# Performance work log

Measured on AMD Instinct MI355X. Metric: run time of the kernel, lower is better.

Reference implementation:

```python
import jax, jax.numpy as jnp
import numpy as np

STRIDES = (8, 16, 32, 64, 128)
NUM_CLASSES = 80
TOPK = 1000
CONF_THRESH = 0.05
NMS_THRESH = 0.6
IMG_H = IMG_W = 2048
CLASS_OFFSET = 100000.0  # > any box coordinate, makes different-class boxes disjoint


def _level_decode(cls, reg, ctn, scale, stride):
    # cls: [1,C,H,W], reg: [1,4,H,W], ctn: [1,1,H,W]
    C, H, W = cls.shape[1], cls.shape[2], cls.shape[3]
    cls = jnp.transpose(cls[0], (1, 2, 0)).reshape(-1, C)       # [HW, C]
    reg = jnp.transpose(reg[0], (1, 2, 0)).reshape(-1, 4)       # [HW, 4]
    reg = jax.nn.relu(reg * scale) * stride                      # Scale + relu + stride
    ctn = jnp.transpose(ctn[0], (1, 2, 0)).reshape(-1, 1)       # [HW, 1]
    prob = jnp.sqrt(jax.nn.sigmoid(cls) * jax.nn.sigmoid(ctn))  # [HW, C]
    scores = prob.max(axis=-1)
    labels = prob.argmax(axis=-1)
    ys, xs = jnp.meshgrid(jnp.arange(H), jnp.arange(W), indexing='ij')
    anchors = (jnp.stack([xs, ys], axis=-1).reshape(-1, 2).astype(cls.dtype) + 0.5) * stride
    if scores.shape[0] > TOPK:
        scores, idx = jax.lax.top_k(scores, TOPK)
        labels, reg, anchors = labels[idx], reg[idx], anchors[idx]
    # decode (l,t,r,b) deltas around anchor centers -> (x1,y1,x2,y2)
    boxes = jnp.concatenate([anchors - reg[:, :2], anchors + reg[:, 2:]], axis=-1)
    return scores, labels, boxes


def _nms_keep(boxes, scores, valid, thresh):
    # Sequential greedy NMS, same math as the numpy loop in RTEFCOS.nms.
    order = jnp.argsort(-jnp.where(valid, scores, -jnp.inf))
    b = boxes[order]
    v = valid[order]
    x1, y1, x2, y2 = b[:, 0], b[:, 1], b[:, 2], b[:, 3]
    areas = (x2 - x1) * (y2 - y1)
    n = b.shape[0]
    pos = jnp.arange(n)

    def body(i, keep):
        xx1 = jnp.maximum(x1[i], x1)
        yy1 = jnp.maximum(y1[i], y1)
        xx2 = jnp.minimum(x2[i], x2)
        yy2 = jnp.minimum(y2[i], y2)
        inter = jnp.maximum(1e-10, xx2 - xx1) * jnp.maximum(1e-10, yy2 - yy1)
        ovr = inter / (areas[i] + areas - inter + 1e-14)
        suppress = (ovr > thresh) & (pos > i) & keep[i]
        return keep & (~suppress)

    keep_sorted = jax.lax.fori_loop(0, n, body, v)
    return jnp.zeros(n, dtype=bool).at[order].set(keep_sorted)


def reference(cls0, reg0, ctn0, cls1, reg1, ctn1, cls2, reg2, ctn2,
              cls3, reg3, ctn3, cls4, reg4, ctn4, scales):
    levels = [(cls0, reg0, ctn0), (cls1, reg1, ctn1), (cls2, reg2, ctn2),
              (cls3, reg3, ctn3), (cls4, reg4, ctn4)]
    all_s, all_l, all_b = [], [], []
    for lv, (c, r, t) in enumerate(levels):
        s, l, b = _level_decode(c, r, t, scales[lv], STRIDES[lv])
        all_s.append(s); all_l.append(l); all_b.append(b)
    scores = jnp.concatenate(all_s)   # [M]
    labels = jnp.concatenate(all_l)   # [M]
    bboxes = jnp.concatenate(all_b)   # [M, 4]
    valid = scores >= CONF_THRESH     # conf filter as mask (static shapes)
    # class-wise NMS via coordinate-offset trick: boxes of different classes
    # never overlap, so one greedy pass == per-class greedy passes.
    boxes_off = bboxes + labels[:, None].astype(bboxes.dtype) * CLASS_OFFSET
    keep = _nms_keep(boxes_off, scores, valid, NMS_THRESH)
    bboxes = bboxes / jnp.array([IMG_W, IMG_H, IMG_W, IMG_H], dtype=bboxes.dtype)
    bboxes = jnp.clip(bboxes, 0.0, 1.0)
    return bboxes, scores, labels, keep


def setup_inputs():
    key = jax.random.key(0)
    ks = jax.random.split(key, len(STRIDES))
    inp = {}
    for lv, stride in enumerate(STRIDES):
        H = IMG_H // stride
        W = IMG_W // stride
        k1, k2, k3 = jax.random.split(ks[lv], 3)
        inp[f"cls{lv}"] = jax.random.normal(k1, (1, NUM_CLASSES, H, W), jnp.float32)
        inp[f"reg{lv}"] = jax.random.uniform(k2, (1, 4, H, W), jnp.float32)
        inp[f"ctn{lv}"] = jax.random.normal(k3, (1, 1, H, W), jnp.float32)
    inp["scales"] = jnp.ones((5,), jnp.float32)
    return inp
```

## Files before the change

### kernel.cpp

```cpp
#include <hip/hip_runtime.h>
#include <math.h>

#define TOTAL_ANCHORS 87296
#define NTOPK 87040
#define NSEL 4256
#define NWORDS 67
#define NPAD   4288
#define MAXROUNDS 4300
#define CANDMAX 8192
#define NBIN 32768
#define NSLAB 8

__device__ __forceinline__ float sigmoidf_(float x) {
    return 1.0f / (1.0f + expf(-x));
}
__device__ __forceinline__ unsigned int f2s(float f) {
    unsigned int u = __float_as_uint(f);
    return u ^ ((u >> 31) ? 0xFFFFFFFFu : 0x80000000u);
}
__device__ __forceinline__ float s2f(unsigned int k) {
    unsigned int u = (k & 0x80000000u) ? (k ^ 0x80000000u) : ~k;
    return __uint_as_float(u);
}
__device__ __forceinline__ void level_of(int g, int& lv, int& base, int& W, int& stride) {
    if (g < 65536)      { lv = 0; base = 0;     W = 256; stride = 8;   }
    else if (g < 81920) { lv = 1; base = 65536; W = 128; stride = 16;  }
    else if (g < 86016) { lv = 2; base = 81920; W = 64;  stride = 32;  }
    else if (g < 87040) { lv = 3; base = 86016; W = 32;  stride = 64;  }
    else                { lv = 4; base = 87040; W = 16;  stride = 128; }
}

struct InPtrs {
    const float* cls[5];
    const float* reg[5];
    const float* ctn[5];
    const float* scales;
};

__global__ __launch_bounds__(256) void cmax_kernel(InPtrs in,
        unsigned long long* __restrict__ cmax2) {
    int a = blockIdx.x * 256 + threadIdx.x;
    int cg = blockIdx.y;
    int lv, base, W, stride;
    level_of(a, lv, base, W, stride);
    (void)stride;
    int p = a - base;
    int HW = W * W;
    const float* cls = in.cls[lv];
    float sctn = sigmoidf_(in.ctn[lv][p]);
    int c0 = cg * 8;
    float v[8];
    #pragma unroll
    for (int k = 0; k < 8; ++k) v[k] = cls[(c0 + k) * HW + p];
    unsigned long long best = 0ull;
    #pragma unroll
    for (int k = 0; k < 8; ++k) {
        float pr = sqrtf(__fmul_rn(sigmoidf_(v[k]), sctn));
        unsigned long long key = ((unsigned long long)f2s(pr) << 32)
                               | (unsigned long long)(255 - (c0 + k));
        best = (key > best) ? key : best;
    }
    cmax2[(size_t)cg * TOTAL_ANCHORS + a] = best;
}

__global__ __launch_bounds__(256) void decode2_kernel(InPtrs in,
        const unsigned long long* __restrict__ cmax2,
        unsigned long long* __restrict__ keys, float* __restrict__ scores,
        int* __restrict__ labels, float4* __restrict__ boxes) {
    int g = blockIdx.x * 256 + threadIdx.x;
    int lv, base, W, stride;
    level_of(g, lv, base, W, stride);
    int p = g - base;
    int HW = W * W;
    int x = p & (W - 1);
    int y = p / W;
    unsigned long long mk = 0ull;
    #pragma unroll
    for (int cg = 0; cg < 10; ++cg) {
        unsigned long long v = cmax2[(size_t)cg * TOTAL_ANCHORS + g];
        mk = (v > mk) ? v : mk;
    }
    float best = s2f((unsigned int)(mk >> 32));
    int lbl = 255 - (int)(mk & 0xFFull);
    float scale = in.scales[lv];
    float fs = (float)stride;
    const float* rg = in.reg[lv];
    float r0 = __fmul_rn(fmaxf(__fmul_rn(rg[0 * HW + p], scale), 0.0f), fs);
    float r1 = __fmul_rn(fmaxf(__fmul_rn(rg[1 * HW + p], scale), 0.0f), fs);
    float r2 = __fmul_rn(fmaxf(__fmul_rn(rg[2 * HW + p], scale), 0.0f), fs);
    float r3 = __fmul_rn(fmaxf(__fmul_rn(rg[3 * HW + p], scale), 0.0f), fs);
    float ax = __fmul_rn(__fadd_rn((float)x, 0.5f), fs);
    float ay = __fmul_rn(__fadd_rn((float)y, 0.5f), fs);
    float4 b;
    b.x = __fsub_rn(ax, r0);
    b.y = __fsub_rn(ay, r1);
    b.z = __fadd_rn(ax, r2);
    b.w = __fadd_rn(ay, r3);
    scores[g] = best;
    labels[g] = lbl;
    boxes[g]  = b;
    keys[g] = (mk & 0xFFFFFFFF00000000ull)
            | (unsigned long long)(unsigned int)(~(unsigned int)p);
}

__global__ __launch_bounds__(1024) void hist_kernel(
        const unsigned long long* __restrict__ keys,
        unsigned int* __restrict__ slab) {
    __shared__ unsigned int h[NBIN / 2];
    const int starts[NSLAB] = {0, 16384, 32768, 49152, 65536, 73728, 81920, 86016};
    const int ends[NSLAB]   = {16384, 32768, 49152, 65536, 73728, 81920, 86016, 87040};
    const int tid = threadIdx.x;
    for (int i = tid; i < NBIN / 2; i += 1024) h[i] = 0u;
    __syncthreads();
    const int s = starts[blockIdx.x], e = ends[blockIdx.x];
    for (int i = s + tid; i < e; i += 1024) {
        unsigned int bin = (unsigned int)(keys[i] >> 48) & 0x7FFFu;
        atomicAdd(&h[bin >> 1], 1u << ((bin & 1u) << 4));
    }
    __syncthreads();
    unsigned int* out = slab + blockIdx.x * (NBIN / 2);
    for (int i = tid; i < NBIN / 2; i += 1024) out[i] = h[i];
}

__global__ __launch_bounds__(1024) void select_kernel(
        const unsigned int* __restrict__ slab, unsigned int* __restrict__ thr,
        unsigned int* __restrict__ cnt) {
    const int lvl = blockIdx.x;
    const int slabS[4] = {0, 4, 6, 7};
    const int slabE[4] = {4, 6, 7, 8};
    const int tid = threadIdx.x;
    if (lvl == 0 && tid < 128) cnt[tid] = 0u;
    __shared__ unsigned int csum[1024];
    unsigned int s = 0;
    for (int sb = slabS[lvl]; sb < slabE[lvl]; ++sb) {
        const unsigned int* A = slab + sb * (NBIN / 2);
        #pragma unroll 4
        for (int w = tid * 16; w < tid * 16 + 16; ++w) {
            unsigned int v = A[w];
            s += (v & 0xFFFFu) + (v >> 16);
        }
    }
    csum[tid] = s;
    __syncthreads();
    for (int off = 1; off < 1024; off <<= 1) {
        unsigned int v = csum[tid] + ((tid + off < 1024) ? csum[tid + off] : 0u);
        __syncthreads();
        csum[tid] = v;
        __syncthreads();
    }
    unsigned int incl = csum[tid];
    unsigned int incl1 = (tid == 1023) ? 0u : csum[tid + 1];
    if (incl >= 1000u && incl1 < 1000u) {
        unsigned int running = incl1;
        for (int b = tid * 32 + 31; b >= tid * 32; --b) {
            unsigned int c = 0;
            for (int sb = slabS[lvl]; sb < slabE[lvl]; ++sb) {
                unsigned int v = slab[sb * (NBIN / 2) + (b >> 1)];
                c += (v >> ((b & 1) << 4)) & 0xFFFFu;
            }
            running += c;
            if (running >= 1000u) { thr[lvl] = (unsigned int)b; break; }
        }
    }
}

__global__ __launch_bounds__(1024) void gather_kernel(
        const unsigned long long* __restrict__ keys,
        const unsigned int* __restrict__ thr,
        unsigned long long* __restrict__ cand, unsigned int* __restrict__ cnt) {
    int g = blockIdx.x * 1024 + threadIdx.x;
    int lvl;
    if (g < 65536)      lvl = 0;
    else if (g < 81920) lvl = 1;
    else if (g < 86016) lvl = 2;
    else                lvl = 3;
    unsigned long long k = keys[g];
    bool pass = (((unsigned int)(k >> 48)) & 0x7FFFu) >= thr[lvl];
    __shared__ unsigned int woff[16];
    __shared__ unsigned int base_;
    const int wave = threadIdx.x >> 6, lane = threadIdx.x & 63;
    unsigned long long m = __ballot(pass);
    if (lane == 0) woff[wave] = (unsigned int)__popcll(m);
    __syncthreads();
    if (threadIdx.x == 0) {
        unsigned int tot = 0;
        #pragma unroll
        for (int w = 0; w < 16; ++w) { unsigned int c = woff[w]; woff[w] = tot; tot += c; }
        base_ = atomicAdd(&cnt[lvl << 5], tot);
    }
    __syncthreads();
    if (pass) {
        unsigned int pos = base_ + woff[wave]
                         + (unsigned int)__popcll(m & ((1ull << lane) - 1ull));
        if (pos < CANDMAX) cand[(lvl << 13) + pos] = k;
    }
}

__global__ __launch_bounds__(1024) void finalsort_kernel(
        const unsigned long long* __restrict__ cand,
        const unsigned int* __restrict__ cnt,
        unsigned long long* __restrict__ sel) {
    const int lvl = blockIdx.x;
    const int tid = threadIdx.x;
    __shared__ unsigned long long sk[CANDMAX];
    int n = (int)cnt[lvl << 5];
    if (n > CANDMAX) n = CANDMAX;
    int P = 1024;
    while (P < n) P <<= 1;
    for (int i = tid; i < P; i += 1024)
        sk[i] = (i < n) ? cand[(lvl << 13) + i] : 0ull;
    __syncthreads();
    for (int kk = 2; kk <= P; kk <<= 1) {
        for (int j = kk >> 1; j > 0; j >>= 1) {
            for (int i = tid; i < P; i += 1024) {
                int ixj = i ^ j;
                if (ixj > i) {
                    unsigned long long a = sk[i], b = sk[ixj];
                    bool sw = ((i & kk) == 0) ? (a < b) : (a > b);
                    if (sw) { sk[i] = b; sk[ixj] = a; }
                }
            }
            __syncthreads();
        }
    }
    if (tid < 1000) sel[lvl * 1000 + tid] = sk[tid];
}

#define PEND_VEC 3216
__global__ __launch_bounds__(256) void fin_kernel(
        const unsigned long long* __restrict__ sel,
        const float* __restrict__ scores, const int* __restrict__ labels,
        const float4* __restrict__ boxes, float* __restrict__ out,
        float4* __restrict__ entbox, float* __restrict__ entarea,
        int* __restrict__ entvalid, unsigned long long* __restrict__ ekeyG,
        float4* __restrict__ pendzero) {
    int pos = blockIdx.x * 256 + threadIdx.x;
    if (pos < PEND_VEC) pendzero[pos] = make_float4(0.f, 0.f, 0.f, 0.f);
    if (pos >= NSEL) return;
    int g;
    if (pos < 4000) {
        int lv = pos / 1000;
        const int offs_[4] = {0, 65536, 81920, 86016};
        unsigned long long key = sel[pos];
        unsigned int p = ~((unsigned int)(key & 0xFFFFFFFFull));
        g = offs_[lv] + (int)p;
    } else {
        g = 87040 + (pos - 4000);
    }
    float sc = scores[g];
    int lb = labels[g];
    float4 bx = boxes[g];
    const float inv = 1.0f / 2048.0f;
    out[pos * 4 + 0] = fminf(fmaxf(__fmul_rn(bx.x, inv), 0.0f), 1.0f);
    out[pos * 4 + 1] = fminf(fmaxf(__fmul_rn(bx.y, inv), 0.0f), 1.0f);
    out[pos * 4 + 2] = fminf(fmaxf(__fmul_rn(bx.z, inv), 0.0f), 1.0f);
    out[pos * 4 + 3] = fminf(fmaxf(__fmul_rn(bx.w, inv), 0.0f), 1.0f);
    out[17024 + pos] = sc;
    out[21280 + pos] = (float)lb;
    out[25536 + pos] = 0.0f;
    float off = __fmul_rn((float)lb, 100000.0f);
    float4 eb;
    eb.x = __fadd_rn(bx.x, off); eb.y = __fadd_rn(bx.y, off);
    eb.z = __fadd_rn(bx.z, off); eb.w = __fadd_rn(bx.w, off);
    entbox[pos] = eb;
    entarea[pos] = __fmul_rn(__fsub_rn(eb.z, eb.x), __fsub_rn(eb.w, eb.y));
    int valid = (sc >= 0.05f) ? 1 : 0;
    entvalid[pos] = valid;
    float effs = valid ? sc : -INFINITY;
    ekeyG[pos] = ((unsigned long long)f2s(effs) << 32) | (unsigned int)(~(unsigned int)pos);
}

__device__ __forceinline__ int count_greater(const unsigned long long* A, int n,
                                             unsigned long long x) {
    int lo = 0, hi = n;
    while (lo < hi) { int m = (lo + hi) >> 1; if (A[m] > x) lo = m + 1; else hi = m; }
    return lo;
}
__global__ __launch_bounds__(1024) void rank_kernel(
        const unsigned long long* __restrict__ ekeyG,
        const float4* __restrict__ entbox, const float* __restrict__ entarea,
        const int* __restrict__ entvalid,
        int* __restrict__ order, float4* __restrict__ sbox,
        float* __restrict__ sarea, int* __restrict__ svalid) {
    __shared__ unsigned long long eL[4000];
    __shared__ unsigned long long sk4[256];
    const int tid = threadIdx.x;
    for (int i = tid; i < 4000; i += 1024) eL[i] = ekeyG[i];
    if (tid < 256) sk4[tid] = ekeyG[4000 + tid];
    __syncthreads();
    for (int kk = 2; kk <= 256; kk <<= 1) {
        for (int j = kk >> 1; j > 0; j >>= 1) {
            if (tid < 256) {
                int ixj = tid ^ j;
                if (ixj > tid) {
                    unsigned long long a = sk4[tid], b = sk4[ixj];
                    bool sw = ((tid & kk) == 0) ? (a < b) : (a > b);
                    if (sw) { sk4[tid] = b; sk4[ixj] = a; }
                }
            }
            __syncthreads();
        }
    }
    int pos = blockIdx.x * 1024 + tid;
    if (pos < NSEL) {
        unsigned long long x = (pos < 4000) ? eL[pos] : ekeyG[pos];
        int rank = count_greater(eL,        1000, x)
                 + count_greater(eL + 1000, 1000, x)
                 + count_greater(eL + 2000, 1000, x)
                 + count_greater(eL + 3000, 1000, x)
                 + count_greater(sk4,        256, x);
        order[rank]  = pos;
        sbox[rank]   = entbox[pos];
        sarea[rank]  = entarea[pos];
        svalid[rank] = entvalid[pos];
    }
}

__global__ __launch_bounds__(64) void mask_kernel(
        const float4* __restrict__ sbox, const float* __restrict__ sarea,
        const int* __restrict__ svalid,
        unsigned long long* __restrict__ maskC,
        unsigned long long* __restrict__ pend0G,
        unsigned int* __restrict__ pend1G) {
    int colTile = blockIdx.x, rowTile = blockIdx.y;
    if (colTile > rowTile) return;
    __shared__ float4 cb[64];
    __shared__ float ca[64];
    int tid = threadIdx.x;
    int col0 = colTile * 64;
    int c = col0 + tid;
    int vcol = 0;
    if (c < NSEL) { cb[tid] = sbox[c]; ca[tid] = sarea[c]; vcol = svalid[c]; }
    else { cb[tid] = make_float4(0.f, 0.f, 0.f, 0.f); ca[tid] = 0.f; }
    unsigned long long unkw = __ballot(vcol != 0);
    __syncthreads();
    int i = rowTile * 64 + tid;
    unsigned long long bits = 0ull;
    if (i < NSEL) {
        float4 b = sbox[i];
        float ar = sarea[i];
        for (int j = 0; j < 64; ++j) {
            float xx1 = fmaxf(b.x, cb[j].x);
            float yy1 = fmaxf(b.y, cb[j].y);
            float xx2 = fminf(b.z, cb[j].z);
            float yy2 = fminf(b.w, cb[j].w);
            float w = fmaxf(1e-10f, __fsub_rn(xx2, xx1));
            float h = fmaxf(1e-10f, __fsub_rn(yy2, yy1));
            float inter = __fmul_rn(w, h);
            float denom = __fadd_rn(__fsub_rn(__fadd_rn(ar, ca[j]), inter), 1e-14f);
            float ovr = __fdiv_rn(inter, denom);
            if (ovr > 0.6f) bits |= (1ull << j);
        }
    }
    maskC[(size_t)colTile * NPAD + i] = bits;
    if (colTile < rowTile && i < NSEL && (bits & unkw)) {
        if (colTile < 64) atomicOr(&pend0G[i], 1ull << colTile);
        else              atomicOr(&pend1G[i], 1u << (colTile - 64));
    }
}

__global__ __launch_bounds__(1024) void sweep_kernel(
        const unsigned long long* __restrict__ maskC,
        const unsigned long long* __restrict__ pend0G,
        const unsigned int* __restrict__ pend1G,
        const int* __restrict__ order, const int* __restrict__ svalid,
        float* __restrict__ out_keep) {
    const int tid = threadIdx.x;
    const int lane = tid & 63;
    const int wave = tid >> 6;
    __shared__ unsigned long long keptL[NWORDS], unkL[NWORDS];
    __shared__ unsigned long long nk[NWORDS], nkC[NWORDS], ndC[NWORDS];
    __shared__ unsigned long long cm0s;
    __shared__ unsigned int cm1s;
    __shared__ int anych;
    __shared__ int wflag[16];

    unsigned long long md[5], pend0[5];
    unsigned int pendH[5];
    #pragma unroll
    for (int k = 0; k < 5; ++k) {
        int b = wave + 16 * k;
        unsigned long long w = 0ull;
        md[k] = 0ull; pend0[k] = 0ull; pendH[k] = 0u;
        if (b < NWORDS) {
            int c = b * 64 + lane;
            int v = (c < NSEL) ? svalid[c] : 0;
            w = __ballot(v != 0);
            md[k]    = maskC[(size_t)b * NPAD + c];
            pend0[k] = pend0G[c];
            pendH[k] = pend1G[c];
            if (lane == 0) { unkL[b] = w; keptL[b] = 0ull; nk[b] = 0ull; }
        }
    }
    if (tid == 0) { cm0s = 0ull; cm1s = 0u; }
    __syncthreads();

    for (int round = 0; round < MAXROUNDS; ++round) {
        unsigned long long cm0 = cm0s;
        unsigned int cm1 = cm1s;
        #pragma unroll
        for (int k = 0; k < 5; ++k) {
            int b = wave + 16 * k;
            bool kp = false, dec = false;
            if (b < NWORDS) {
                int c = b * 64 + lane;
                unsigned long long uw = unkL[b];
                if ((uw >> lane) & 1ull) {
                    bool rem = false;
                    unsigned long long todo = pend0[k] & cm0;
                    while (todo) {
                        int w = __ffsll((long long)todo) - 1;
                        todo &= todo - 1ull;
                        unsigned long long m = maskC[(size_t)w * NPAD + c];
                        if (m & nk[w]) { rem = true; break; }
                        if ((m & unkL[w]) == 0ull) pend0[k] &= ~(1ull << w);
                    }
                    if (!rem) {
                        unsigned int todoH = pendH[k] & cm1;
                        while (todoH) {
                            int bit = __ffs(todoH) - 1;
                            todoH &= todoH - 1u;
                            int w = 64 + bit;
                            unsigned long long m = maskC[(size_t)w * NPAD + c];
                            if (m & nk[w]) { rem = true; break; }
                            if ((m & unkL[w]) == 0ull) pendH[k] &= ~(1u << bit);
                        }
                    }
                    unsigned long long below = (1ull << lane) - 1ull;
                    if (!rem && (md[k] & keptL[b] & below)) rem = true;
                    if (!rem && pend0[k] == 0ull && pendH[k] == 0u
                             && (md[k] & uw & below) == 0ull) kp = true;
                    dec = rem || kp;
                }
            }
            unsigned long long kb = __ballot(kp);
            unsigned long long db = __ballot(dec);
            if (b < NWORDS && lane == 0) { nkC[b] = kb; ndC[b] = db; }
        }
        __syncthreads();
        int any = 0;
        #pragma unroll
        for (int k = 0; k < 5; ++k) {
            int b = wave + 16 * k;
            if (b >= NWORDS) continue;
            unsigned long long db = ndC[b];
            if (lane == 0) {
                keptL[b] |= nkC[b];
                unkL[b]  &= ~db;
                nk[b]     = nkC[b];
            }
            any |= (db != 0ull) ? 1 : 0;
        }
        if (lane == 0) wflag[wave] = any;
        __syncthreads();
        if (tid == 0) {
            unsigned long long c0 = 0ull; unsigned int c1 = 0u; int a = 0;
            for (int w = 0; w < 64; ++w) if (ndC[w]) c0 |= (1ull << w);
            for (int w = 64; w < NWORDS; ++w) if (ndC[w]) c1 |= (1u << (w - 64));
            #pragma unroll
            for (int w = 0; w < 16; ++w) a |= wflag[w];
            cm0s = c0; cm1s = c1; anych = a;
        }
        __syncthreads();
        if (!anych) break;
    }

    #pragma unroll
    for (int k = 0; k < 5; ++k) {
        int b = wave + 16 * k;
        if (b >= NWORDS) continue;
        int c = b * 64 + lane;
        if (c < NSEL && ((keptL[b] >> lane) & 1ull)) out_keep[order[c]] = 1.0f;
    }
}

constexpr size_t OFF_KEYS    = 0;
constexpr size_t OFF_SCORES  = OFF_KEYS    + 698368;
constexpr size_t OFF_LABELS  = OFF_SCORES  + 349184;
constexpr size_t OFF_BOXES   = OFF_LABELS  + 349184;
constexpr size_t OFF_SEL     = OFF_BOXES   + 1396736;
constexpr size_t OFF_ORDER   = OFF_SEL     + 32000;
constexpr size_t OFF_SBOX    = OFF_ORDER   + 17024;
constexpr size_t OFF_SAREA   = OFF_SBOX    + 68096;
constexpr size_t OFF_SVALID  = OFF_SAREA   + 17024;
constexpr size_t OFF_MASK    = OFF_SVALID  + 17024;
constexpr size_t OFF_CMAX2   = OFF_MASK    + (size_t)NWORDS * NPAD * 8;
constexpr size_t OFF_CNT     = OFF_CMAX2   + 10u * 698368u;
constexpr size_t OFF_PEND0   = OFF_CNT     + 512;
constexpr size_t OFF_PEND1   = OFF_PEND0   + (size_t)NPAD * 8;
constexpr size_t OFF_THR     = OFF_PEND1   + (size_t)NPAD * 4;
constexpr size_t OFF_SLAB    = OFF_THR     + 64;
constexpr size_t OFF_CAND    = OFF_SLAB    + (size_t)NSLAB * 16384u * 4u;
constexpr size_t OFF_EKEY    = OFF_CAND    + 4u * CANDMAX * 8u;
constexpr size_t OFF_ENTBOX  = OFF_EKEY    + 34048;
constexpr size_t OFF_ENTAREA = OFF_ENTBOX  + 68096;
constexpr size_t OFF_ENTVAL  = OFF_ENTAREA + 17024;

extern "C" void kernel_launch(void* const* d_in, const int* in_sizes, int n_in,
                              void* d_out, int out_size, void* d_ws, size_t ws_size,
                              hipStream_t stream) {
    (void)in_sizes; (void)n_in; (void)out_size; (void)ws_size;
    InPtrs P;
    for (int lv = 0; lv < 5; ++lv) {
        P.cls[lv] = (const float*)d_in[3 * lv + 0];
        P.reg[lv] = (const float*)d_in[3 * lv + 1];
        P.ctn[lv] = (const float*)d_in[3 * lv + 2];
    }
    P.scales = (const float*)d_in[15];

    char* ws = (char*)d_ws;
    unsigned long long* keys   = (unsigned long long*)(ws + OFF_KEYS);
    float*              scores = (float*)             (ws + OFF_SCORES);
    int*                labels = (int*)               (ws + OFF_LABELS);
    float4*             boxes  = (float4*)            (ws + OFF_BOXES);
    unsigned long long* sel    = (unsigned long long*)(ws + OFF_SEL);
    int*                order  = (int*)               (ws + OFF_ORDER);
    float4*             sbox   = (float4*)            (ws + OFF_SBOX);
    float*              sarea  = (float*)             (ws + OFF_SAREA);
    int*                svalid = (int*)               (ws + OFF_SVALID);
    unsigned long long* maskb  = (unsigned long long*)(ws + OFF_MASK);
    unsigned long long* cmax2  = (unsigned long long*)(ws + OFF_CMAX2);
    unsigned int*       cnt    = (unsigned int*)      (ws + OFF_CNT);
    unsigned long long* pend0  = (unsigned long long*)(ws + OFF_PEND0);
    unsigned int*       pend1  = (unsigned int*)      (ws + OFF_PEND1);
    unsigned int*       thr    = (unsigned int*)      (ws + OFF_THR);
    unsigned int*       slab   = (unsigned int*)      (ws + OFF_SLAB);
    unsigned long long* cand   = (unsigned long long*)(ws + OFF_CAND);
    unsigned long long* ekeyG  = (unsigned long long*)(ws + OFF_EKEY);
    float4*             entbox = (float4*)            (ws + OFF_ENTBOX);
    float*              entarea= (float*)             (ws + OFF_ENTAREA);
    int*                entval = (int*)               (ws + OFF_ENTVAL);
    float* out = (float*)d_out;

    cmax_kernel<<<dim3(341, 10), 256, 0, stream>>>(P, cmax2);
    decode2_kernel<<<341, 256, 0, stream>>>(P, cmax2, keys, scores, labels, boxes);
    hist_kernel<<<NSLAB, 1024, 0, stream>>>(keys, slab);
    select_kernel<<<4, 1024, 0, stream>>>(slab, thr, cnt);
    gather_kernel<<<85, 1024, 0, stream>>>(keys, thr, cand, cnt);
    finalsort_kernel<<<4, 1024, 0, stream>>>(cand, cnt, sel);
    fin_kernel<<<(NSEL + 255) / 256, 256, 0, stream>>>(sel, scores, labels, boxes, out,
                                                       entbox, entarea, entval, ekeyG,
                                                       (float4*)(ws + OFF_PEND0));
    rank_kernel<<<(NSEL + 1023) / 1024, 1024, 0, stream>>>(ekeyG, entbox, entarea, entval,
                                                           order, sbox, sarea, svalid);
    mask_kernel<<<dim3(NWORDS, NWORDS), 64, 0, stream>>>(sbox, sarea, svalid,
                                                         maskb, pend0, pend1);
    sweep_kernel<<<1, 1024, 0, stream>>>(maskb, pend0, pend1, order, svalid, out + 25536);
}
```

Before: 120.8 us.

## Fuse threshold select, candidate gather and bitonic sort into one kernel

Merges the select, gather and final-sort kernels into a single per-level block that finds the histogram threshold, compacts passing keys into shared memory with wave-level atomics, and bitonic-sorts them there. This removes two kernel launches and the global candidate buffer, counter and threshold round-trips. In exchange, only 4 blocks scan all 87k keys instead of 85 blocks, so the gather phase has much less parallelism. Candidate capacity also drops slightly to fit metadata in the 64KB of shared memory.

```diff
diff --git a/kernel.cpp b/kernel.cpp
--- a/kernel.cpp
+++ b/kernel.cpp
@@ -7,9 +7,10 @@
 #define NWORDS 67
 #define NPAD   4288
 #define MAXROUNDS 4300
-#define CANDMAX 8192
+#define CANDCAP 8190
 #define NBIN 32768
 #define NSLAB 8
+#define PEND_VEC 3216
 
 __device__ __forceinline__ float sigmoidf_(float x) {
     return 1.0f / (1.0f + expf(-x));
@@ -122,15 +123,18 @@
     for (int i = tid; i < NBIN / 2; i += 1024) out[i] = h[i];
 }
 
-__global__ __launch_bounds__(1024) void select_kernel(
-        const unsigned int* __restrict__ slab, unsigned int* __restrict__ thr,
-        unsigned int* __restrict__ cnt) {
+__global__ __launch_bounds__(1024) void topksel_kernel(
+        const unsigned long long* __restrict__ keys,
+        const unsigned int* __restrict__ slab,
+        unsigned long long* __restrict__ sel) {
     const int lvl = blockIdx.x;
+    const int tid = threadIdx.x;
+    __shared__ __align__(16) unsigned char sm[65536];
+    unsigned int* csum = (unsigned int*)sm;
+    unsigned int* meta = (unsigned int*)sm;
+    unsigned long long* cand = (unsigned long long*)(sm + 16);
     const int slabS[4] = {0, 4, 6, 7};
     const int slabE[4] = {4, 6, 7, 8};
-    const int tid = threadIdx.x;
-    if (lvl == 0 && tid < 128) cnt[tid] = 0u;
-    __shared__ unsigned int csum[1024];
     unsigned int s = 0;
     for (int sb = slabS[lvl]; sb < slabE[lvl]; ++sb) {
         const unsigned int* A = slab + sb * (NBIN / 2);
@@ -150,6 +154,8 @@
     }
     unsigned int incl = csum[tid];
     unsigned int incl1 = (tid == 1023) ? 0u : csum[tid + 1];
+    __syncthreads();
+    if (tid == 0) meta[1] = 0u;
     if (incl >= 1000u && incl1 < 1000u) {
         unsigned int running = incl1;
         for (int b = tid * 32 + 31; b >= tid * 32; --b) {
@@ -159,74 +165,53 @@
                 c += (v >> ((b & 1) << 4)) & 0xFFFFu;
             }
             running += c;
-            if (running >= 1000u) { thr[lvl] = (unsigned int)b; break; }
-        }
-    }
-}
-
-__global__ __launch_bounds__(1024) void gather_kernel(
-        const unsigned long long* __restrict__ keys,
-        const unsigned int* __restrict__ thr,
-        unsigned long long* __restrict__ cand, unsigned int* __restrict__ cnt) {
-    int g = blockIdx.x * 1024 + threadIdx.x;
-    int lvl;
-    if (g < 65536)      lvl = 0;
-    else if (g < 81920) lvl = 1;
-    else if (g < 86016) lvl = 2;
-    else                lvl = 3;
-    unsigned long long k = keys[g];
-    bool pass = (((unsigned int)(k >> 48)) & 0x7FFFu) >= thr[lvl];
-    __shared__ unsigned int woff[16];
-    __shared__ unsigned int base_;
-    const int wave = threadIdx.x >> 6, lane = threadIdx.x & 63;
-    unsigned long long m = __ballot(pass);
-    if (lane == 0) woff[wave] = (unsigned int)__popcll(m);
-    __syncthreads();
-    if (threadIdx.x == 0) {
-        unsigned int tot = 0;
-        #pragma unroll
-        for (int w = 0; w < 16; ++w) { unsigned int c = woff[w]; woff[w] = tot; tot += c; }
-        base_ = atomicAdd(&cnt[lvl << 5], tot);
-    }
-    __syncthreads();
-    if (pass) {
-        unsigned int pos = base_ + woff[wave]
-                         + (unsigned int)__popcll(m & ((1ull << lane) - 1ull));
-        if (pos < CANDMAX) cand[(lvl << 13) + pos] = k;
-    }
-}
-
-__global__ __launch_bounds__(1024) void finalsort_kernel(
-        const unsigned long long* __restrict__ cand,
-        const unsigned int* __restrict__ cnt,
-        unsigned long long* __restrict__ sel) {
-    const int lvl = blockIdx.x;
-    const int tid = threadIdx.x;
-    __shared__ unsigned long long sk[CANDMAX];
-    int n = (int)cnt[lvl << 5];
-    if (n > CANDMAX) n = CANDMAX;
+            if (running >= 1000u) { meta[0] = (unsigned int)b; break; }
+        }
+    }
+    __syncthreads();
+    const unsigned int T = meta[0];
+    const int startsL[4] = {0, 65536, 81920, 86016};
+    const int endsL[4]   = {65536, 81920, 86016, 87040};
+    const int lane = tid & 63;
+    for (int i = startsL[lvl] + tid; i < endsL[lvl]; i += 1024) {
+        unsigned long long k = keys[i];
+        bool pass = (((unsigned int)(k >> 48)) & 0x7FFFu) >= T;
+        unsigned long long mm = __ballot(pass);
+        if (mm) {
+            int leader = __ffsll((long long)mm) - 1;
+            unsigned int base_ = 0;
+            if (lane == leader) base_ = atomicAdd(&meta[1], (unsigned int)__popcll(mm));
+            base_ = (unsigned int)__shfl((int)base_, leader);
+            if (pass) {
+                unsigned int pos = base_ + (unsigned int)__popcll(mm & ((1ull << lane) - 1ull));
+                if (pos < CANDCAP) cand[pos] = k;
+            }
+        }
+    }
+    __syncthreads();
+    int n = (int)meta[1];
+    if (n > CANDCAP) n = CANDCAP;
     int P = 1024;
     while (P < n) P <<= 1;
-    for (int i = tid; i < P; i += 1024)
-        sk[i] = (i < n) ? cand[(lvl << 13) + i] : 0ull;
+    if (P > CANDCAP) P = 8192;
+    for (int i = tid; i < P; i += 1024) if (i >= n) { if (i < CANDCAP) cand[i] = 0ull; }
     __syncthreads();
     for (int kk = 2; kk <= P; kk <<= 1) {
         for (int j = kk >> 1; j > 0; j >>= 1) {
             for (int i = tid; i < P; i += 1024) {
                 int ixj = i ^ j;
-                if (ixj > i) {
-                    unsigned long long a = sk[i], b = sk[ixj];
+                if (ixj > i && ixj < CANDCAP && i < CANDCAP) {
+                    unsigned long long a = cand[i], b = cand[ixj];
                     bool sw = ((i & kk) == 0) ? (a < b) : (a > b);
-                    if (sw) { sk[i] = b; sk[ixj] = a; }
+                    if (sw) { cand[i] = b; cand[ixj] = a; }
                 }
             }
             __syncthreads();
         }
     }
-    if (tid < 1000) sel[lvl * 1000 + tid] = sk[tid];
-}
-
-#define PEND_VEC 3216
+    if (tid < 1000) sel[lvl * 1000 + tid] = cand[tid];
+}
+
 __global__ __launch_bounds__(256) void fin_kernel(
         const unsigned long long* __restrict__ sel,
         const float* __restrict__ scores, const int* __restrict__ labels,
@@ -485,13 +470,10 @@
 constexpr size_t OFF_SVALID  = OFF_SAREA   + 17024;
 constexpr size_t OFF_MASK    = OFF_SVALID  + 17024;
 constexpr size_t OFF_CMAX2   = OFF_MASK    + (size_t)NWORDS * NPAD * 8;
-constexpr size_t OFF_CNT     = OFF_CMAX2   + 10u * 698368u;
-constexpr size_t OFF_PEND0   = OFF_CNT     + 512;
+constexpr size_t OFF_PEND0   = OFF_CMAX2   + 10u * 698368u;
 constexpr size_t OFF_PEND1   = OFF_PEND0   + (size_t)NPAD * 8;
-constexpr size_t OFF_THR     = OFF_PEND1   + (size_t)NPAD * 4;
-constexpr size_t OFF_SLAB    = OFF_THR     + 64;
-constexpr size_t OFF_CAND    = OFF_SLAB    + (size_t)NSLAB * 16384u * 4u;
-constexpr size_t OFF_EKEY    = OFF_CAND    + 4u * CANDMAX * 8u;
+constexpr size_t OFF_SLAB    = OFF_PEND1   + (size_t)NPAD * 4;
+constexpr size_t OFF_EKEY    = OFF_SLAB    + (size_t)NSLAB * 16384u * 4u;
 constexpr size_t OFF_ENTBOX  = OFF_EKEY    + 34048;
 constexpr size_t OFF_ENTAREA = OFF_ENTBOX  + 68096;
 constexpr size_t OFF_ENTVAL  = OFF_ENTAREA + 17024;
@@ -520,12 +502,9 @@
     int*                svalid = (int*)               (ws + OFF_SVALID);
     unsigned long long* maskb  = (unsigned long long*)(ws + OFF_MASK);
     unsigned long long* cmax2  = (unsigned long long*)(ws + OFF_CMAX2);
-    unsigned int*       cnt    = (unsigned int*)      (ws + OFF_CNT);
     unsigned long long* pend0  = (unsigned long long*)(ws + OFF_PEND0);
     unsigned int*       pend1  = (unsigned int*)      (ws + OFF_PEND1);
-    unsigned int*       thr    = (unsigned int*)      (ws + OFF_THR);
     unsigned int*       slab   = (unsigned int*)      (ws + OFF_SLAB);
-    unsigned long long* cand   = (unsigned long long*)(ws + OFF_CAND);
     unsigned long long* ekeyG  = (unsigned long long*)(ws + OFF_EKEY);
     float4*             entbox = (float4*)            (ws + OFF_ENTBOX);
     float*              entarea= (float*)             (ws + OFF_ENTAREA);
@@ -535,9 +514,7 @@
     cmax_kernel<<<dim3(341, 10), 256, 0, stream>>>(P, cmax2);
     decode2_kernel<<<341, 256, 0, stream>>>(P, cmax2, keys, scores, labels, boxes);
     hist_kernel<<<NSLAB, 1024, 0, stream>>>(keys, slab);
-    select_kernel<<<4, 1024, 0, stream>>>(slab, thr, cnt);
-    gather_kernel<<<85, 1024, 0, stream>>>(keys, thr, cand, cnt);
-    finalsort_kernel<<<4, 1024, 0, stream>>>(cand, cnt, sel);
+    topksel_kernel<<<4, 1024, 0, stream>>>(keys, slab, sel);
     fin_kernel<<<(NSEL + 255) / 256, 256, 0, stream>>>(sel, scores, labels, boxes, out,
                                                        entbox, entarea, entval, ekeyG,
                                                        (float4*)(ws + OFF_PEND0));
```

Result: slower. 143.6 us (+18.9%).
